# Optimization experiments

Measured on AMD Instinct MI355X. Metric: run time of the kernel, lower is better.

Reference implementation:

```python
import jax, jax.numpy as jnp
import numpy as np

B, S, H = 32, 2048, 1024


def setup_inputs() -> dict:
    key = jax.random.key(0)
    k1, k2, k3, k4, k5 = jax.random.split(key, 5)
    # scale linear weights like torch default init (~U(-1/sqrt(fan_in),..)); normal*small is fine for a numeric baseline
    return {
        "hidden": jax.random.normal(k1, (B, H), dtype=jnp.float32),
        "encoder_outputs": jax.random.normal(k2, (B, S, H), dtype=jnp.float32),
        "attn_w": jax.random.normal(k3, (H, 2 * H), dtype=jnp.float32) * (1.0 / np.sqrt(2 * H)),
        "attn_b": jax.random.normal(k4, (H,), dtype=jnp.float32) * (1.0 / np.sqrt(2 * H)),
        "v_w": jax.random.normal(k5, (1, H), dtype=jnp.float32) * (1.0 / np.sqrt(H)),
    }


def reference(hidden, encoder_outputs, attn_w, attn_b, v_w):
    # hidden: [B,H]; encoder_outputs: [B,S,H]
    # torch: cat((hidden repeated over S, enc), dim=2) @ attn_w.T + attn_b
    # Split attn_w columns: first H cols act on hidden, last H cols on enc.
    # Avoids materializing the repeated/concatenated [B,S,2H] tensor.
    Hdim = hidden.shape[-1]
    Wh = attn_w[:, :Hdim]   # [H, H] applied to hidden
    We = attn_w[:, Hdim:]   # [H, H] applied to encoder outputs
    # [B,1,H] + [B,S,H] + [H] -> tanh -> [B,S,H]
    e = jnp.tanh((hidden @ Wh.T)[:, None, :] + jnp.einsum('bsh,kh->bsk', encoder_outputs, We) + attn_b)
    scores = jnp.einsum('bsh,h->bs', e, v_w[0])          # [B,S], v has no bias
    attn_weights = jax.nn.softmax(scores, axis=1)        # softmax over source positions (dim=1)
    context = jnp.einsum('bs,bsh->bh', attn_weights, encoder_outputs)  # [B,H]
    output = jnp.concatenate([context, hidden], axis=1)  # [B,2H]
    return output, attn_weights[..., None]               # match torch shapes: [B,2H], [B,S,1]
```

## Files before the change

### kernel.cpp

```cpp
#include <hip/hip_runtime.h>
#include <stdint.h>

#define BATCH 32
#define SEQ   2048
#define HDIM  1024

typedef short short8 __attribute__((ext_vector_type(8)));
typedef float f32x4 __attribute__((ext_vector_type(4)));

__device__ __forceinline__ unsigned short f2b(float f) {
    unsigned u = __float_as_uint(f);
    u += 0x7FFFu + ((u >> 16) & 1u);
    return (unsigned short)(u >> 16);
}
__device__ __forceinline__ unsigned pk_bf16(float a, float b) {
    return __builtin_amdgcn_perm(__float_as_uint(b), __float_as_uint(a), 0x07060302u);
}
__device__ __forceinline__ float fast_tanh(float x) {
    float ex = __expf(2.0f * x);
    return 1.0f - 2.0f / (ex + 1.0f);
}
__device__ __forceinline__ void gl2lds16(const unsigned short* g, unsigned short* l) {
    __builtin_amdgcn_global_load_lds(
        (const __attribute__((address_space(1))) unsigned int*)g,
        (__attribute__((address_space(3))) unsigned int*)l, 16, 0, 0);
}

__global__ __launch_bounds__(256) void prep_convert_kernel(
    const float* __restrict__ hidden, const float* __restrict__ attn_w,
    const float* __restrict__ attn_b, const float* __restrict__ enc,
    unsigned short* __restrict__ we_bf, unsigned short* __restrict__ enc_bf,
    float* __restrict__ qb, float* __restrict__ scores) {
    int bid = blockIdx.x;
    int tid = threadIdx.x;
    __shared__ float red[4][BATCH];

    if (bid < 2048) {
        int m = bid >> 2, g = bid & 3;
        int r = tid >> 1, h = tid & 1;
        const float* src = enc + ((size_t)m * 128 + r) * HDIM;
        int r7 = r & 7;
#pragma unroll
        for (int k4 = 0; k4 < 4; ++k4) {
            int kt = g * 4 + k4;
            unsigned short* img =
                enc_bf + ((size_t)m * 16 + kt) * 8192 + r * 64 + h * 32;
#pragma unroll
            for (int p = 0; p < 4; ++p) {
                int c = (4 * h + p) ^ r7;
                const float4* s = (const float4*)(src + kt * 64 + c * 8);
                float4 x = s[0], y = s[1];
                uint4 o;
                o.x = pk_bf16(x.x, x.y); o.y = pk_bf16(x.z, x.w);
                o.z = pk_bf16(y.x, y.y); o.w = pk_bf16(y.z, y.w);
                *(uint4*)(img + p * 8) = o;
            }
        }
        return;
    }

    int k = bid - 2048;
    if (tid < 64) scores[(size_t)k * 64 + tid] = 0.0f;

    {
        const float4* src = (const float4*)(attn_w + (size_t)k * 2048 + 1024);
        float4 v = src[tid];
        ushort4 o;
        o.x = f2b(v.x); o.y = f2b(v.y); o.z = f2b(v.z); o.w = f2b(v.w);
        ((ushort4*)(we_bf + (size_t)k * HDIM))[tid] = o;
    }

    float part[BATCH];
#pragma unroll
    for (int b = 0; b < BATCH; ++b) part[b] = 0.0f;
    const float* wrow = attn_w + (size_t)k * 2048;
    for (int h = tid; h < HDIM; h += 256) {
        float w = wrow[h];
#pragma unroll
        for (int b = 0; b < BATCH; ++b) part[b] += w * hidden[b * HDIM + h];
    }
    int lane = tid & 63, wv = tid >> 6;
#pragma unroll
    for (int b = 0; b < BATCH; ++b) {
        float v = part[b];
        v += __shfl_xor(v, 1);  v += __shfl_xor(v, 2);  v += __shfl_xor(v, 4);
        v += __shfl_xor(v, 8);  v += __shfl_xor(v, 16); v += __shfl_xor(v, 32);
        if (lane == 0) red[wv][b] = v;
    }
    __syncthreads();
    if (tid < BATCH) {
        float v = red[0][tid] + red[1][tid] + red[2][tid] + red[3][tid] + attn_b[k];
        qb[(size_t)tid * HDIM + k] = v;
    }
}

__global__ __launch_bounds__(256, 5) void score_gemm_kernel(
    const unsigned short* __restrict__ enc_bf,
    const unsigned short* __restrict__ we_bf,
    const float* __restrict__ qb, const float* __restrict__ v_w,
    float* __restrict__ scores) {
    __shared__ __align__(16) unsigned short As[8192];
    __shared__ __align__(16) unsigned short Bs[8192];

    int tid  = threadIdx.x;
    int lane = tid & 63, w = tid >> 6;
    int wm = w & 1, wn = w >> 1;
    int i15 = lane & 15, q = lane >> 4;

    int raw   = blockIdx.x;
    int i     = raw >> 3;
    int ntile = i & 7;
    int mtile = (raw & 7) * 64 + (i >> 3);
    int n0 = ntile * 128;
    long gm0 = (long)mtile * 128;
    int b = mtile >> 4;

    int brow_in = lane >> 3;
    int bchunk  = (lane & 7) ^ ((lane >> 3) & 7);
    const unsigned short* Bg =
        we_bf + (size_t)(n0 + w * 32 + brow_in) * HDIM + bchunk * 8;
    unsigned short* Bd = Bs + (w * 32) * 64 + lane * 8;

    const unsigned short* Atile = enc_bf + (size_t)mtile * 16 * 8192;
    int aoff = w * 2048 + lane * 8;

    f32x4 acc[4][4];
#pragma unroll
    for (int mt = 0; mt < 4; ++mt)
#pragma unroll
        for (int nt = 0; nt < 4; ++nt) acc[mt][nt] = (f32x4)0.0f;

    int arow0 = wm * 64 + i15;
    int brow0 = wn * 64 + i15;

#define STAGE(KT) do {                                                        \
        const unsigned short* bsrc = Bg + (size_t)(KT) * 64;                  \
        gl2lds16(bsrc,                     Bd);                               \
        gl2lds16(bsrc + (size_t)8  * HDIM, Bd + 512);                         \
        gl2lds16(bsrc + (size_t)16 * HDIM, Bd + 1024);                        \
        gl2lds16(bsrc + (size_t)24 * HDIM, Bd + 1536);                        \
        const unsigned short* asrc = Atile + (size_t)(KT) * 8192 + aoff;      \
        unsigned short* adst = As + aoff;                                     \
        gl2lds16(asrc,        adst);                                          \
        gl2lds16(asrc + 512,  adst + 512);                                    \
        gl2lds16(asrc + 1024, adst + 1024);                                   \
        gl2lds16(asrc + 1536, adst + 1536);                                   \
    } while (0)

    STAGE(0);
    __syncthreads();

    for (int kt = 0; kt < 16; ++kt) {
#pragma unroll
        for (int kk = 0; kk < 2; ++kk) {
            int xr = ((kk * 4 + q) ^ (i15 & 7)) * 8;
            short8 af[4], bf[4];
#pragma unroll
            for (int mt = 0; mt < 4; ++mt)
                af[mt] = *(const short8*)(As + (arow0 + mt * 16) * 64 + xr);
#pragma unroll
            for (int nt = 0; nt < 4; ++nt)
                bf[nt] = *(const short8*)(Bs + (brow0 + nt * 16) * 64 + xr);
#pragma unroll
            for (int mt = 0; mt < 4; ++mt)
#pragma unroll
                for (int nt = 0; nt < 4; ++nt)
                    acc[mt][nt] = __builtin_amdgcn_mfma_f32_16x16x32_bf16(
                        af[mt], bf[nt], acc[mt][nt], 0, 0, 0);
        }
        if (kt < 15) {
            __syncthreads();
            STAGE(kt + 1);
            __syncthreads();
        }
    }
#undef STAGE

    float sc[4][4];
#pragma unroll
    for (int mt = 0; mt < 4; ++mt)
#pragma unroll
        for (int r = 0; r < 4; ++r) sc[mt][r] = 0.0f;

#pragma unroll
    for (int nt = 0; nt < 4; ++nt) {
        int n = n0 + wn * 64 + nt * 16 + i15;
        float qv = qb[(size_t)b * HDIM + n];
        float vv = v_w[n];
#pragma unroll
        for (int mt = 0; mt < 4; ++mt)
#pragma unroll
            for (int r = 0; r < 4; ++r)
                sc[mt][r] += vv * fast_tanh(acc[mt][nt][r] + qv);
    }
#pragma unroll
    for (int mt = 0; mt < 4; ++mt)
#pragma unroll
        for (int r = 0; r < 4; ++r) {
            float v = sc[mt][r];
            v += __shfl_xor(v, 1); v += __shfl_xor(v, 2);
            v += __shfl_xor(v, 4); v += __shfl_xor(v, 8);
            if (i15 == 0)
                atomicAdd(&scores[gm0 + wm * 64 + mt * 16 + q * 4 + r], v);
        }
}

__global__ __launch_bounds__(256) void softmax_stats_kernel(
    const float* __restrict__ scores, const float* __restrict__ hidden,
    float* __restrict__ stats, float* out) {
    int b = blockIdx.x, tid = threadIdx.x;
    const float* srow = scores + (size_t)b * SEQ;
    __shared__ float redm[4];
    __shared__ float reds[4];
    int lane = tid & 63, wv = tid >> 6;

    float loc[8];
    float m = -1e30f;
#pragma unroll
    for (int i = 0; i < 8; ++i) {
        loc[i] = srow[tid + i * 256];
        m = fmaxf(m, loc[i]);
    }
#pragma unroll
    for (int d = 1; d < 64; d <<= 1) m = fmaxf(m, __shfl_xor(m, d));
    if (lane == 0) redm[wv] = m;
    __syncthreads();
    m = fmaxf(fmaxf(redm[0], redm[1]), fmaxf(redm[2], redm[3]));

    float sum = 0.0f;
#pragma unroll
    for (int i = 0; i < 8; ++i) sum += __expf(loc[i] - m);
#pragma unroll
    for (int d = 1; d < 64; d <<= 1) sum += __shfl_xor(sum, d);
    if (lane == 0) reds[wv] = sum;
    __syncthreads();
    if (tid == 0) {
        float s = reds[0] + reds[1] + reds[2] + reds[3];
        stats[2 * b]     = m;
        stats[2 * b + 1] = 1.0f / s;
    }

    for (int i = tid; i < HDIM; i += 256) {
        out[(size_t)b * 2048 + i] = 0.0f;
        out[(size_t)b * 2048 + 1024 + i] = hidden[(size_t)b * HDIM + i];
    }
}

__global__ __launch_bounds__(256) void context_kernel(
    const float* __restrict__ enc, const float* __restrict__ scores,
    const float* __restrict__ stats, float* out) {
    int id = blockIdx.x;
    int scid = id & 15, b = id >> 4;
    int tid = threadIdx.x;
    __shared__ float wl[128];
    float m = stats[2 * b], inv = stats[2 * b + 1];
    if (tid < 128) {
        float s = scores[(size_t)b * SEQ + scid * 128 + tid];
        float wgt = __expf(s - m) * inv;
        wl[tid] = wgt;
        out[BATCH * SEQ + (size_t)b * SEQ + scid * 128 + tid] = wgt;
    }
    __syncthreads();
    const float* ebase = enc + ((size_t)(b * SEQ + scid * 128)) * HDIM + tid * 4;
    float a0 = 0.f, a1 = 0.f, a2 = 0.f, a3 = 0.f;
    float b0 = 0.f, b1 = 0.f, b2 = 0.f, b3 = 0.f;
#pragma unroll 4
    for (int s = 0; s < 64; ++s) {
        float4 e0 = *(const float4*)(ebase + (size_t)s * HDIM);
        float4 e1 = *(const float4*)(ebase + (size_t)(s + 64) * HDIM);
        float w0 = wl[s], w1 = wl[s + 64];
        a0 += w0 * e0.x; a1 += w0 * e0.y; a2 += w0 * e0.z; a3 += w0 * e0.w;
        b0 += w1 * e1.x; b1 += w1 * e1.y; b2 += w1 * e1.z; b3 += w1 * e1.w;
    }
    float* o = out + (size_t)b * 2048 + tid * 4;
    atomicAdd(o + 0, a0 + b0); atomicAdd(o + 1, a1 + b1);
    atomicAdd(o + 2, a2 + b2); atomicAdd(o + 3, a3 + b3);
}

extern "C" void kernel_launch(void* const* d_in, const int* in_sizes, int n_in,
                              void* d_out, int out_size, void* d_ws, size_t ws_size,
                              hipStream_t stream) {
    const float* hidden = (const float*)d_in[0];
    const float* enc    = (const float*)d_in[1];
    const float* attn_w = (const float*)d_in[2];
    const float* attn_b = (const float*)d_in[3];
    const float* v_w    = (const float*)d_in[4];
    float* out = (float*)d_out;

    char* ws = (char*)d_ws;
    unsigned short* enc_bf = (unsigned short*)ws;
    unsigned short* we_bf  = (unsigned short*)(ws + (size_t)134217728);
    float* qb     = (float*)(ws + (size_t)134217728 + 2097152);
    float* scores = (float*)(ws + (size_t)134217728 + 2097152 + 131072);
    float* stats  = (float*)(ws + (size_t)134217728 + 2097152 + 131072 + 262144);

    prep_convert_kernel<<<3072, 256, 0, stream>>>(hidden, attn_w, attn_b, enc,
                                                  we_bf, enc_bf, qb, scores);
    score_gemm_kernel<<<4096, 256, 0, stream>>>(enc_bf, we_bf, qb, v_w, scores);
    softmax_stats_kernel<<<32, 256, 0, stream>>>(scores, hidden, stats, out);
    context_kernel<<<512, 256, 0, stream>>>(enc, scores, stats, out);
}
```

Measured before the change: 630.6 us.

## Double-buffer GEMM LDS, fuse softmax stats into context, coalesce enc conversion

The score GEMM now keeps two LDS buffers and prefetches the next K tile while computing the current one. This drops one barrier per iteration and raises wave priority around the MFMA block. The softmax stats kernel is removed: each context block recomputes the row max and sum itself, and the zero/hidden copy into the output moves into extra blocks of the prep kernel. The enc-to-bf16 conversion is rewritten so that reads are coalesced row by row. The costs are doubled LDS use per block (launch bound lowered to 2 blocks per SU), redundant per-block reductions over each score row, and one fewer kernel launch.

```diff
diff --git a/kernel.cpp b/kernel.cpp
--- a/kernel.cpp
+++ b/kernel.cpp
@@ -30,32 +30,40 @@
     const float* __restrict__ hidden, const float* __restrict__ attn_w,
     const float* __restrict__ attn_b, const float* __restrict__ enc,
     unsigned short* __restrict__ we_bf, unsigned short* __restrict__ enc_bf,
-    float* __restrict__ qb, float* __restrict__ scores) {
+    float* __restrict__ qb, float* __restrict__ scores, float* out) {
     int bid = blockIdx.x;
     int tid = threadIdx.x;
     __shared__ float red[4][BATCH];
 
     if (bid < 2048) {
         int m = bid >> 2, g = bid & 3;
-        int r = tid >> 1, h = tid & 1;
-        const float* src = enc + ((size_t)m * 128 + r) * HDIM;
-        int r7 = r & 7;
-#pragma unroll
-        for (int k4 = 0; k4 < 4; ++k4) {
-            int kt = g * 4 + k4;
-            unsigned short* img =
-                enc_bf + ((size_t)m * 16 + kt) * 8192 + r * 64 + h * 32;
-#pragma unroll
-            for (int p = 0; p < 4; ++p) {
-                int c = (4 * h + p) ^ r7;
-                const float4* s = (const float4*)(src + kt * 64 + c * 8);
-                float4 x = s[0], y = s[1];
-                uint4 o;
-                o.x = pk_bf16(x.x, x.y); o.y = pk_bf16(x.z, x.w);
-                o.z = pk_bf16(y.x, y.y); o.w = pk_bf16(y.z, y.w);
-                *(uint4*)(img + p * 8) = o;
-            }
+        int wv = tid >> 6, l = tid & 63;
+        int ktl   = l >> 4;
+        int cpair = (l & 15) >> 1;
+        int half  = l & 1;
+        const float* srcbase = enc + (size_t)m * 128 * HDIM + g * 256 + l * 4;
+        unsigned short* imgk =
+            enc_bf + ((size_t)m * 16 + g * 4 + ktl) * 8192 + half * 4;
+#pragma unroll 4
+        for (int it = 0; it < 32; ++it) {
+            int r = it * 4 + wv;
+            float4 v = *(const float4*)(srcbase + (size_t)r * HDIM);
+            uint2 o;
+            o.x = pk_bf16(v.x, v.y);
+            o.y = pk_bf16(v.z, v.w);
+            int p = cpair ^ (r & 7);
+            *(uint2*)(imgk + r * 64 + p * 8) = o;
         }
+        return;
+    }
+
+    if (bid >= 3072) {
+        int b = bid - 3072;
+        float4* dz = (float4*)(out + (size_t)b * 2048);
+        const float4* hs = (const float4*)(hidden + (size_t)b * HDIM);
+        float4 z; z.x = z.y = z.z = z.w = 0.0f;
+        dz[tid] = z;
+        dz[256 + tid] = hs[tid];
         return;
     }
 
@@ -94,13 +102,13 @@
     }
 }
 
-__global__ __launch_bounds__(256, 5) void score_gemm_kernel(
+__global__ __launch_bounds__(256, 2) void score_gemm_kernel(
     const unsigned short* __restrict__ enc_bf,
     const unsigned short* __restrict__ we_bf,
     const float* __restrict__ qb, const float* __restrict__ v_w,
     float* __restrict__ scores) {
-    __shared__ __align__(16) unsigned short As[8192];
-    __shared__ __align__(16) unsigned short Bs[8192];
+    __shared__ __align__(16) unsigned short As[2 * 8192];
+    __shared__ __align__(16) unsigned short Bs[2 * 8192];
 
     int tid  = threadIdx.x;
     int lane = tid & 63, w = tid >> 6;
@@ -119,7 +127,7 @@
     int bchunk  = (lane & 7) ^ ((lane >> 3) & 7);
     const unsigned short* Bg =
         we_bf + (size_t)(n0 + w * 32 + brow_in) * HDIM + bchunk * 8;
-    unsigned short* Bd = Bs + (w * 32) * 64 + lane * 8;
+    int bdoff = (w * 32) * 64 + lane * 8;
 
     const unsigned short* Atile = enc_bf + (size_t)mtile * 16 * 8192;
     int aoff = w * 2048 + lane * 8;
@@ -133,34 +141,41 @@
     int arow0 = wm * 64 + i15;
     int brow0 = wn * 64 + i15;
 
-#define STAGE(KT) do {                                                        \
+#define STAGE(KT, BUF) do {                                                   \
+        unsigned short* Bd = Bs + (BUF) * 8192 + bdoff;                       \
         const unsigned short* bsrc = Bg + (size_t)(KT) * 64;                  \
         gl2lds16(bsrc,                     Bd);                               \
         gl2lds16(bsrc + (size_t)8  * HDIM, Bd + 512);                         \
         gl2lds16(bsrc + (size_t)16 * HDIM, Bd + 1024);                        \
         gl2lds16(bsrc + (size_t)24 * HDIM, Bd + 1536);                        \
         const unsigned short* asrc = Atile + (size_t)(KT) * 8192 + aoff;      \
-        unsigned short* adst = As + aoff;                                     \
+        unsigned short* adst = As + (BUF) * 8192 + aoff;                      \
         gl2lds16(asrc,        adst);                                          \
         gl2lds16(asrc + 512,  adst + 512);                                    \
         gl2lds16(asrc + 1024, adst + 1024);                                   \
         gl2lds16(asrc + 1536, adst + 1536);                                   \
     } while (0)
 
-    STAGE(0);
+    STAGE(0, 0);
     __syncthreads();
 
     for (int kt = 0; kt < 16; ++kt) {
+        int cur = kt & 1;
+        if (kt < 15) STAGE(kt + 1, cur ^ 1);
+
+        const unsigned short* Ac = As + cur * 8192;
+        const unsigned short* Bc = Bs + cur * 8192;
+        __builtin_amdgcn_s_setprio(1);
 #pragma unroll
         for (int kk = 0; kk < 2; ++kk) {
             int xr = ((kk * 4 + q) ^ (i15 & 7)) * 8;
             short8 af[4], bf[4];
 #pragma unroll
             for (int mt = 0; mt < 4; ++mt)
-                af[mt] = *(const short8*)(As + (arow0 + mt * 16) * 64 + xr);
+                af[mt] = *(const short8*)(Ac + (arow0 + mt * 16) * 64 + xr);
 #pragma unroll
             for (int nt = 0; nt < 4; ++nt)
-                bf[nt] = *(const short8*)(Bs + (brow0 + nt * 16) * 64 + xr);
+                bf[nt] = *(const short8*)(Bc + (brow0 + nt * 16) * 64 + xr);
 #pragma unroll
             for (int mt = 0; mt < 4; ++mt)
 #pragma unroll
@@ -168,11 +183,9 @@
                     acc[mt][nt] = __builtin_amdgcn_mfma_f32_16x16x32_bf16(
                         af[mt], bf[nt], acc[mt][nt], 0, 0, 0);
         }
-        if (kt < 15) {
-            __syncthreads();
-            STAGE(kt + 1);
-            __syncthreads();
-        }
+        __builtin_amdgcn_s_setprio(0);
+
+        if (kt < 15) __syncthreads();
     }
 #undef STAGE
 
@@ -205,13 +218,16 @@
         }
 }
 
-__global__ __launch_bounds__(256) void softmax_stats_kernel(
-    const float* __restrict__ scores, const float* __restrict__ hidden,
-    float* __restrict__ stats, float* out) {
-    int b = blockIdx.x, tid = threadIdx.x;
+__global__ __launch_bounds__(256) void context_kernel(
+    const float* __restrict__ enc, const float* __restrict__ scores,
+    float* out) {
+    int id = blockIdx.x;
+    int scid = id & 15, b = id >> 4;
+    int tid = threadIdx.x;
     const float* srow = scores + (size_t)b * SEQ;
     __shared__ float redm[4];
     __shared__ float reds[4];
+    __shared__ float wl[128];
     int lane = tid & 63, wv = tid >> 6;
 
     float loc[8];
@@ -234,33 +250,16 @@
     for (int d = 1; d < 64; d <<= 1) sum += __shfl_xor(sum, d);
     if (lane == 0) reds[wv] = sum;
     __syncthreads();
-    if (tid == 0) {
-        float s = reds[0] + reds[1] + reds[2] + reds[3];
-        stats[2 * b]     = m;
-        stats[2 * b + 1] = 1.0f / s;
-    }
-
-    for (int i = tid; i < HDIM; i += 256) {
-        out[(size_t)b * 2048 + i] = 0.0f;
-        out[(size_t)b * 2048 + 1024 + i] = hidden[(size_t)b * HDIM + i];
-    }
-}
-
-__global__ __launch_bounds__(256) void context_kernel(
-    const float* __restrict__ enc, const float* __restrict__ scores,
-    const float* __restrict__ stats, float* out) {
-    int id = blockIdx.x;
-    int scid = id & 15, b = id >> 4;
-    int tid = threadIdx.x;
-    __shared__ float wl[128];
-    float m = stats[2 * b], inv = stats[2 * b + 1];
+    float inv = 1.0f / (reds[0] + reds[1] + reds[2] + reds[3]);
+
     if (tid < 128) {
-        float s = scores[(size_t)b * SEQ + scid * 128 + tid];
+        float s = srow[scid * 128 + tid];
         float wgt = __expf(s - m) * inv;
         wl[tid] = wgt;
         out[BATCH * SEQ + (size_t)b * SEQ + scid * 128 + tid] = wgt;
     }
     __syncthreads();
+
     const float* ebase = enc + ((size_t)(b * SEQ + scid * 128)) * HDIM + tid * 4;
     float a0 = 0.f, a1 = 0.f, a2 = 0.f, a3 = 0.f;
     float b0 = 0.f, b1 = 0.f, b2 = 0.f, b3 = 0.f;
@@ -292,11 +291,9 @@
     unsigned short* we_bf  = (unsigned short*)(ws + (size_t)134217728);
     float* qb     = (float*)(ws + (size_t)134217728 + 2097152);
     float* scores = (float*)(ws + (size_t)134217728 + 2097152 + 131072);
-    float* stats  = (float*)(ws + (size_t)134217728 + 2097152 + 131072 + 262144);
-
-    prep_convert_kernel<<<3072, 256, 0, stream>>>(hidden, attn_w, attn_b, enc,
-                                                  we_bf, enc_bf, qb, scores);
+
+    prep_convert_kernel<<<3104, 256, 0, stream>>>(hidden, attn_w, attn_b, enc,
+                                                  we_bf, enc_bf, qb, scores, out);
     score_gemm_kernel<<<4096, 256, 0, stream>>>(enc_bf, we_bf, qb, v_w, scores);
-    softmax_stats_kernel<<<32, 256, 0, stream>>>(scores, hidden, stats, out);
-    context_kernel<<<512, 256, 0, stream>>>(enc, scores, stats, out);
-}
+    context_kernel<<<512, 256, 0, stream>>>(enc, scores, out);
+}
```

New measurement: 663.4 us. 5.2% more time.
